# Kernel tuning notes

Measured on AMD Instinct MI355X. Metric: run time of the kernel, lower is better.

## Reference

```python
import jax, jax.numpy as jnp
import numpy as np

B, S, L, C, H, D, CP = 32, 4, 64, 32, 4, 8, 16  # batch, tracks, bins, c_msa, heads, d_head, c_pair


def _ln(x, g, b, eps=1e-5):
    m = jnp.mean(x, axis=-1, keepdims=True)
    v = jnp.mean((x - m) ** 2, axis=-1, keepdims=True)
    return (x - m) / jnp.sqrt(v + eps) * g + b


def setup_inputs() -> dict:
    key = jax.random.key(0)
    ks = jax.random.split(key, 20)
    n = lambda k, shape, s=0.1: jax.random.normal(k, shape, jnp.float32) * s
    return dict(
        chip_ctcf=n(ks[0], (B, L), 1.0),
        chip_hac=n(ks[1], (B, L), 1.0),
        chip_me1=n(ks[2], (B, L), 1.0),
        chip_me3=n(ks[3], (B, L), 1.0),
        bulk_map=n(ks[4], (B, 1, L, L), 1.0),
        we_w=n(ks[5], (C, 1)), we_b=jnp.zeros((C,), jnp.float32),
        pos=n(ks[6], (1, 1, L, C)),
        mn_g=jnp.ones((C,), jnp.float32), mn_b=jnp.zeros((C,), jnp.float32),
        wq=n(ks[7], (C, C)), bq=jnp.zeros((C,), jnp.float32),
        wk=n(ks[8], (C, C)), bk=jnp.zeros((C,), jnp.float32),
        wv=n(ks[9], (C, C)), bv=jnp.zeros((C,), jnp.float32),
        wo=n(ks[10], (C, C)), bo=jnp.zeros((C,), jnp.float32),
        an_g=jnp.ones((C,), jnp.float32), an_b=jnp.zeros((C,), jnp.float32),
        conv_w=n(ks[11], (H,)), conv_b=jnp.zeros((H,), jnp.float32),
        gate_w=n(ks[12], (H, D, D)), gate_b=jnp.zeros((H, D), jnp.float32),
        pp_w=n(ks[13], (CP, C * C), 0.03), pp_b=jnp.zeros((CP,), jnp.float32),
        ada_g=jnp.ones((CP,), jnp.float32), ada_b=jnp.zeros((CP,), jnp.float32),
        ada_alpha=jnp.ones((1,), jnp.float32),
    )


def reference(chip_ctcf, chip_hac, chip_me1, chip_me3, bulk_map,
              we_w, we_b, pos, mn_g, mn_b,
              wq, bq, wk, bk, wv, bv, wo, bo, an_g, an_b,
              conv_w, conv_b, gate_w, gate_b,
              pp_w, pp_b, ada_g, ada_b, ada_alpha):
    # 1) build MSA: (B, S=4, L, C)
    signals = jnp.stack([chip_ctcf, chip_hac, chip_me1, chip_me3], axis=1)  # (B,S,L)
    msa = signals[..., None] * we_w[:, 0] + we_b                            # Linear(1,C)
    x = _ln(msa + pos, mn_g, mn_b)                                          # (B,S,L,C)

    # 2) row self-attention with bulk-derived per-head bias
    q = (x @ wq.T + bq).reshape(B, S, L, H, D)
    k = (x @ wk.T + bk).reshape(B, S, L, H, D)
    v = (x @ wv.T + bv).reshape(B, S, L, H, D)
    scores = jnp.einsum('bslhd,bsmhd->bshlm', q, k) / jnp.sqrt(jnp.float32(D))
    bias = bulk_map * conv_w.reshape(1, H, 1, 1) + conv_b.reshape(1, H, 1, 1)  # 1x1 conv -> (B,H,L,L)
    attn = jax.nn.softmax(scores + bias[:, None], axis=-1)                     # (B,S,H,L,L)
    out = jnp.einsum('bshlm,bsmhd->bshld', attn, v)
    gate = jax.nn.sigmoid(jnp.einsum('hcd,bshld->bshlc', gate_w, out)
                          + gate_b[None, None, :, None, :])
    out = out * gate
    out = out.transpose(0, 1, 3, 2, 4).reshape(B, S, L, C)
    out = out @ wo.T + bo
    x = _ln(x + out, an_g, an_b)                                            # post-attn LayerNorm

    # 3) outer-product (of max over tracks) pair features
    m = jnp.max(x, axis=1)                                                  # (B,L,C)
    pair = jnp.einsum('bic,bjd->bijcd', m, m).reshape(B, L, L, C * C)       # (B,L,L,1024)
    nrm = jnp.sqrt(jnp.sum(pair * pair, axis=-1, keepdims=True))
    pair = pair / jnp.maximum(nrm, 1e-6)                                    # F.normalize
    feat = pair @ pp_w.T + pp_b                                             # (B,L,L,CP)
    feat = feat + ada_alpha * _ln(feat, ada_g, ada_b)                       # AdaNorm
    feat = jax.nn.silu(feat)
    return feat.transpose(0, 3, 1, 2)                                       # (B,CP,L,L)
```

## Files before the change

### kernel.cpp

```cpp
#include <hip/hip_runtime.h>
#include <hip/hip_bf16.h>

#define NB 32
#define NS 4
#define NL 64
#define NC 32
#define NH 4
#define ND 8
#define NCP 16

using fp = const float* __restrict__;

__global__ __launch_bounds__(256) void k1_attn(
    fp ctcf, fp hac, fp me1, fp me3, fp bulk,
    fp we_w, fp we_b, fp pos, fp mn_g, fp mn_b,
    fp wq, fp bq, fp wk, fp bk, fp wv, fp bv,
    fp wo, fp bo, fp an_g, fp an_b,
    fp conv_w, fp conv_b, fp gate_w, fp gate_b,
    float* __restrict__ xpostT)
{
    __shared__ float ks_s[NC*NL];
    __shared__ float vs_s[NC*NL];
    __shared__ float ao_s[NC*NL];
    __shared__ float bulk_s[NL*65];
    __shared__ float red1[256], red2[256];

    const int t = threadIdx.x;
    const int w = t >> 6;
    const int l = t & 63;
    const int b = blockIdx.x >> 2;
    const int s = blockIdx.x & 3;

    for (int idx = t; idx < NL*NL; idx += 256)
        bulk_s[(idx >> 6)*65 + (idx & 63)] = bulk[b*NL*NL + idx];

    fp sigp = (s == 0) ? ctcf : (s == 1) ? hac : (s == 2) ? me1 : me3;
    const float sig = sigp[b*NL + l];

    float x[NC];
    float mean = 0.f;
#pragma unroll
    for (int c = 0; c < NC; c++){
        x[c] = sig * we_w[c] + we_b[c] + pos[l*NC + c];
        mean += x[c];
    }
    mean *= (1.f/NC);
    float var = 0.f;
#pragma unroll
    for (int c = 0; c < NC; c++){ float d = x[c] - mean; var += d*d; }
    var *= (1.f/NC);
    float inv = rsqrtf(var + 1e-5f);
#pragma unroll
    for (int c = 0; c < NC; c++) x[c] = (x[c] - mean)*inv*mn_g[c] + mn_b[c];

    float q[ND];
#pragma unroll
    for (int e8 = 0; e8 < ND; e8++){
        int e = w*ND + e8;
        float aq = bq[e], ak = bk[e], av = bv[e];
#pragma unroll
        for (int c = 0; c < NC; c++){
            float xv = x[c];
            aq += xv * wq[e*NC + c];
            ak += xv * wk[e*NC + c];
            av += xv * wv[e*NC + c];
        }
        q[e8] = aq;
        ks_s[e*NL + l] = ak;
        vs_s[e*NL + l] = av;
    }
    __syncthreads();

    const float rs8 = 0.35355339059327373f;
    const float cw = conv_w[w], cb = conv_b[w];
    float srow[NL];
    float mx = -1e30f;
    for (int m = 0; m < NL; m++){
        float dot = 0.f;
#pragma unroll
        for (int d = 0; d < ND; d++)
            dot += q[d] * ks_s[(w*ND + d)*NL + m];
        float v = dot*rs8 + bulk_s[l*65 + m]*cw + cb;
        srow[m] = v;
        mx = fmaxf(mx, v);
    }
    float sm = 0.f;
    for (int m = 0; m < NL; m++){ srow[m] = __expf(srow[m] - mx); sm += srow[m]; }
    float is = 1.f / sm;
    float o[ND];
#pragma unroll
    for (int d = 0; d < ND; d++) o[d] = 0.f;
    for (int m = 0; m < NL; m++){
        float a = srow[m] * is;
#pragma unroll
        for (int d = 0; d < ND; d++)
            o[d] += a * vs_s[(w*ND + d)*NL + m];
    }
#pragma unroll
    for (int c8 = 0; c8 < ND; c8++){
        float g = gate_b[w*ND + c8];
#pragma unroll
        for (int d = 0; d < ND; d++) g += gate_w[(w*ND + c8)*ND + d] * o[d];
        ao_s[(w*ND + c8)*NL + l] = o[c8] * (1.f/(1.f + __expf(-g)));
    }
    __syncthreads();

    float p8[ND];
    float psum = 0.f, psq = 0.f;
#pragma unroll
    for (int c8 = 0; c8 < ND; c8++){
        int c = w*ND + c8;
        float a = bo[c];
#pragma unroll
        for (int e = 0; e < NC; e++) a += ao_s[e*NL + l] * wo[c*NC + e];
        float val = x[c] + a;
        p8[c8] = val; psum += val; psq += val*val;
    }
    red1[w*64 + l] = psum;
    red2[w*64 + l] = psq;
    __syncthreads();
    float sum = 0.f, ssq = 0.f;
#pragma unroll
    for (int ww = 0; ww < 4; ww++){ sum += red1[ww*64 + l]; ssq += red2[ww*64 + l]; }
    mean = sum * (1.f/NC);
    var  = ssq * (1.f/NC) - mean*mean;
    inv  = rsqrtf(var + 1e-5f);
#pragma unroll
    for (int c8 = 0; c8 < ND; c8++){
        int c = w*ND + c8;
        xpostT[((b*NS + s)*NC + c)*NL + l] = (p8[c8] - mean)*inv*an_g[c] + an_b[c];
    }
}

__global__ __launch_bounds__(256) void k2_z(
    const float* __restrict__ xpostT, fp pp_w, float* __restrict__ z)
{
    const int b  = blockIdx.x >> 2;
    const int pg = blockIdx.x & 3;
    const int w  = threadIdx.x >> 6;
    const int j  = threadIdx.x & 63;
    const int p  = pg*4 + w;

    float md[NC];
    float sq = 0.f;
#pragma unroll
    for (int c = 0; c < NC; c++){
        const float* xp = xpostT + (b*NS*NC + c)*NL + j;
        float v = xp[0];
        v = fmaxf(v, xp[NC*NL]);
        v = fmaxf(v, xp[2*NC*NL]);
        v = fmaxf(v, xp[3*NC*NL]);
        md[c] = v; sq += v*v;
    }
    float inv = 1.f / fmaxf(sqrtf(sq), 1e-3f);
#pragma unroll
    for (int c = 0; c < NC; c++) md[c] *= inv;

    fp wrow = pp_w + p*NC*NC;
    for (int c = 0; c < NC; c++){
        float acc = 0.f;
#pragma unroll
        for (int d = 0; d < NC; d++) acc += wrow[c*NC + d] * md[d];
        z[b*NCP*NC*NL + p*NC*NL + c*NL + j] = acc;
    }
}

__global__ __launch_bounds__(256) void k3_out(
    const float* __restrict__ xpostT, const float* __restrict__ z,
    fp pp_b, fp ada_g, fp ada_b, fp ada_alpha,
    float* __restrict__ out)
{
    __shared__ float mh[NC*NL];
    const int b  = blockIdx.x >> 4;
    const int it = blockIdx.x & 15;
    const int t  = threadIdx.x;
    const int w  = t >> 6;
    const int j  = t & 63;

    if (w == 0){
        float m[NC]; float sq = 0.f;
#pragma unroll
        for (int c = 0; c < NC; c++){
            const float* xp = xpostT + (b*NS*NC + c)*NL + j;
            float v = xp[0];
            v = fmaxf(v, xp[NC*NL]);
            v = fmaxf(v, xp[2*NC*NL]);
            v = fmaxf(v, xp[3*NC*NL]);
            m[c] = v; sq += v*v;
        }
        float iv = 1.f / fmaxf(sqrtf(sq), 1e-3f);
#pragma unroll
        for (int c = 0; c < NC; c++) mh[c*NL + j] = m[c]*iv;
    }
    __syncthreads();

    const int i = it*4 + w;

    float mi[NC];
#pragma unroll
    for (int c = 0; c < NC; c++) mi[c] = mh[c*NL + i];

    float acc[NCP];
    const float* zb = z + b*NCP*NC*NL;
#pragma unroll 1
    for (int p = 0; p < NCP; p++){
        float a = 0.f;
#pragma unroll
        for (int c = 0; c < NC; c++)
            a += mi[c] * zb[p*NC*NL + c*NL + j];
        acc[p] = a;
    }

    const float alpha = ada_alpha[0];
    float fsum = 0.f, fsq = 0.f;
#pragma unroll
    for (int p = 0; p < NCP; p++){
        float v = acc[p] + pp_b[p];
        acc[p] = v; fsum += v; fsq += v*v;
    }
    float fmean = fsum * (1.f/NCP);
    float fvar  = fsq * (1.f/NCP) - fmean*fmean;
    float finv  = rsqrtf(fvar + 1e-5f);
#pragma unroll
    for (int p = 0; p < NCP; p++){
        float v = acc[p] + alpha * ((acc[p] - fmean)*finv*ada_g[p] + ada_b[p]);
        out[((b*NCP + p)*NL + i)*NL + j] = v / (1.f + __expf(-v));
    }
}

extern "C" void kernel_launch(void* const* d_in, const int* in_sizes, int n_in,
                              void* d_out, int out_size, void* d_ws, size_t ws_size,
                              hipStream_t stream)
{
    float* ws     = (float*)d_ws;
    float* xpostT = ws;
    float* z      = xpostT + NB*NS*NC*NL;

    k1_attn<<<NB*NS, 256, 0, stream>>>(
        (fp)d_in[0], (fp)d_in[1], (fp)d_in[2], (fp)d_in[3], (fp)d_in[4],
        (fp)d_in[5], (fp)d_in[6], (fp)d_in[7], (fp)d_in[8], (fp)d_in[9],
        (fp)d_in[10], (fp)d_in[11], (fp)d_in[12], (fp)d_in[13], (fp)d_in[14], (fp)d_in[15],
        (fp)d_in[16], (fp)d_in[17], (fp)d_in[18], (fp)d_in[19],
        (fp)d_in[20], (fp)d_in[21], (fp)d_in[22], (fp)d_in[23], xpostT);

    k2_z<<<NB*4, 256, 0, stream>>>(xpostT, (fp)d_in[24], z);

    k3_out<<<NB*16, 256, 0, stream>>>(
        xpostT, z, (fp)d_in[25], (fp)d_in[26], (fp)d_in[27], (fp)d_in[28],
        (float*)d_out);
}
```

Measured before the change: 161.5 us.

## Fuse pair projection kernels by contracting pp_w with row vector first

Merges the z-precompute and output kernels into one. Each block now contracts pp_w with the normalized max-row vectors of its 4 rows into a small shared buffer u (p, i, d), and each thread then dots u with its own column vector. This removes one launch and the global round trip through the z workspace. In exchange every block recomputes the column vector for every thread and reads all of pp_w (64 KB) per block, 512 blocks in total.

```diff
diff --git a/kernel.cpp b/kernel.cpp
--- a/kernel.cpp
+++ b/kernel.cpp
@@ -132,53 +132,23 @@
     }
 }
 
-__global__ __launch_bounds__(256) void k2_z(
-    const float* __restrict__ xpostT, fp pp_w, float* __restrict__ z)
-{
-    const int b  = blockIdx.x >> 2;
-    const int pg = blockIdx.x & 3;
-    const int w  = threadIdx.x >> 6;
-    const int j  = threadIdx.x & 63;
-    const int p  = pg*4 + w;
-
-    float md[NC];
-    float sq = 0.f;
-#pragma unroll
-    for (int c = 0; c < NC; c++){
-        const float* xp = xpostT + (b*NS*NC + c)*NL + j;
-        float v = xp[0];
-        v = fmaxf(v, xp[NC*NL]);
-        v = fmaxf(v, xp[2*NC*NL]);
-        v = fmaxf(v, xp[3*NC*NL]);
-        md[c] = v; sq += v*v;
-    }
-    float inv = 1.f / fmaxf(sqrtf(sq), 1e-3f);
-#pragma unroll
-    for (int c = 0; c < NC; c++) md[c] *= inv;
-
-    fp wrow = pp_w + p*NC*NC;
-    for (int c = 0; c < NC; c++){
-        float acc = 0.f;
-#pragma unroll
-        for (int d = 0; d < NC; d++) acc += wrow[c*NC + d] * md[d];
-        z[b*NCP*NC*NL + p*NC*NL + c*NL + j] = acc;
-    }
-}
-
-__global__ __launch_bounds__(256) void k3_out(
-    const float* __restrict__ xpostT, const float* __restrict__ z,
+__global__ __launch_bounds__(256) void k23_pair(
+    const float* __restrict__ xpostT, fp pp_w,
     fp pp_b, fp ada_g, fp ada_b, fp ada_alpha,
     float* __restrict__ out)
 {
     __shared__ float mh[NC*NL];
+    __shared__ float u[NCP*4*NC];
+
     const int b  = blockIdx.x >> 4;
     const int it = blockIdx.x & 15;
     const int t  = threadIdx.x;
     const int w  = t >> 6;
     const int j  = t & 63;
 
-    if (w == 0){
-        float m[NC]; float sq = 0.f;
+    float md[NC];
+    {
+        float sq = 0.f;
 #pragma unroll
         for (int c = 0; c < NC; c++){
             const float* xp = xpostT + (b*NS*NC + c)*NL + j;
@@ -186,44 +156,57 @@
             v = fmaxf(v, xp[NC*NL]);
             v = fmaxf(v, xp[2*NC*NL]);
             v = fmaxf(v, xp[3*NC*NL]);
-            m[c] = v; sq += v*v;
+            md[c] = v; sq += v*v;
         }
         float iv = 1.f / fmaxf(sqrtf(sq), 1e-3f);
 #pragma unroll
-        for (int c = 0; c < NC; c++) mh[c*NL + j] = m[c]*iv;
-    }
-    __syncthreads();
-
-    const int i = it*4 + w;
-
-    float mi[NC];
-#pragma unroll
-    for (int c = 0; c < NC; c++) mi[c] = mh[c*NL + i];
-
-    float acc[NCP];
-    const float* zb = z + b*NCP*NC*NL;
+        for (int c = 0; c < NC; c++) md[c] *= iv;
+        if (w == 0){
+#pragma unroll
+            for (int c = 0; c < NC; c++) mh[c*NL + j] = md[c];
+        }
+    }
+    __syncthreads();
+
+#pragma unroll
+    for (int loop = 0; loop < 8; loop++){
+        int idx = loop*256 + t;
+        int d  = idx & 31;
+        int ip = (idx >> 5) & 3;
+        int p  = idx >> 7;
+        int i  = it*4 + ip;
+        float acc = 0.f;
+#pragma unroll
+        for (int c = 0; c < NC; c++)
+            acc += mh[c*NL + i] * pp_w[p*NC*NC + c*NC + d];
+        u[idx] = acc;
+    }
+    __syncthreads();
+
+    float f[NCP];
 #pragma unroll 1
     for (int p = 0; p < NCP; p++){
         float a = 0.f;
 #pragma unroll
-        for (int c = 0; c < NC; c++)
-            a += mi[c] * zb[p*NC*NL + c*NL + j];
-        acc[p] = a;
+        for (int d = 0; d < NC; d++)
+            a += u[p*4*NC + w*NC + d] * md[d];
+        f[p] = a;
     }
 
     const float alpha = ada_alpha[0];
     float fsum = 0.f, fsq = 0.f;
 #pragma unroll
     for (int p = 0; p < NCP; p++){
-        float v = acc[p] + pp_b[p];
-        acc[p] = v; fsum += v; fsq += v*v;
+        float v = f[p] + pp_b[p];
+        f[p] = v; fsum += v; fsq += v*v;
     }
     float fmean = fsum * (1.f/NCP);
     float fvar  = fsq * (1.f/NCP) - fmean*fmean;
     float finv  = rsqrtf(fvar + 1e-5f);
+    const int i = it*4 + w;
 #pragma unroll
     for (int p = 0; p < NCP; p++){
-        float v = acc[p] + alpha * ((acc[p] - fmean)*finv*ada_g[p] + ada_b[p]);
+        float v = f[p] + alpha * ((f[p] - fmean)*finv*ada_g[p] + ada_b[p]);
         out[((b*NCP + p)*NL + i)*NL + j] = v / (1.f + __expf(-v));
     }
 }
@@ -232,9 +215,7 @@
                               void* d_out, int out_size, void* d_ws, size_t ws_size,
                               hipStream_t stream)
 {
-    float* ws     = (float*)d_ws;
-    float* xpostT = ws;
-    float* z      = xpostT + NB*NS*NC*NL;
+    float* xpostT = (float*)d_ws;
 
     k1_attn<<<NB*NS, 256, 0, stream>>>(
         (fp)d_in[0], (fp)d_in[1], (fp)d_in[2], (fp)d_in[3], (fp)d_in[4],
@@ -243,9 +224,7 @@
         (fp)d_in[16], (fp)d_in[17], (fp)d_in[18], (fp)d_in[19],
         (fp)d_in[20], (fp)d_in[21], (fp)d_in[22], (fp)d_in[23], xpostT);
 
-    k2_z<<<NB*4, 256, 0, stream>>>(xpostT, (fp)d_in[24], z);
-
-    k3_out<<<NB*16, 256, 0, stream>>>(
-        xpostT, z, (fp)d_in[25], (fp)d_in[26], (fp)d_in[27], (fp)d_in[28],
+    k23_pair<<<NB*16, 256, 0, stream>>>(
+        xpostT, (fp)d_in[24], (fp)d_in[25], (fp)d_in[26], (fp)d_in[27], (fp)d_in[28],
         (float*)d_out);
 }
```

New measurement: 175.1 us. 1.08x slower.
